# Performance work log

Hardware: AMD Instinct MI355X
Metric: run time of the kernel (lower is better)

The kernel has to match this reference:

```python
import jax, jax.numpy as jnp
import numpy as np

NUM_CLASSES = 2   # module init num_classes; class logits have NUM_CLASSES+1 (incl. 'no object')
ORIG_H, ORIG_W = 512, 512  # original input resolution that masks are upsampled to


def setup_inputs() -> dict:
    key = jax.random.key(0)
    k1, k2 = jax.random.split(key)
    B, Q = 8, 100
    h, w = 128, 128  # mask decoder outputs at 1/4 input resolution
    class_queries_logits = jax.random.normal(k1, (B, Q, NUM_CLASSES + 1), dtype=jnp.float32)
    masks_queries_logits = jax.random.normal(k2, (B, Q, h, w), dtype=jnp.float32)
    return {"class_queries_logits": class_queries_logits,
            "masks_queries_logits": masks_queries_logits}


def reference(class_queries_logits, masks_queries_logits):
    B, Q = masks_queries_logits.shape[:2]
    # bilinear upsample to original resolution (align_corners=False == half-pixel centers)
    masks_up = jax.image.resize(masks_queries_logits, (B, Q, ORIG_H, ORIG_W), method="bilinear")
    # softmax over classes (incl. no-object), keep only the first NUM_CLASSES,
    # exactly as the original loop only indexes c in range(num_classes)
    class_probs = jax.nn.softmax(class_queries_logits, axis=-1)[..., :NUM_CLASSES]  # [B,Q,C]
    mask_probs = jax.nn.sigmoid(masks_up)  # [B,Q,H,W]
    # fused replacement for the triple b/q/c Python loop of weighted accumulates
    logits = jnp.einsum("bqc,bqhw->bchw", class_probs, mask_probs)  # [B,C,H,W]
    return logits
```

## Files before the change

kernel.cpp:

```cpp
#include <hip/hip_runtime.h>
#include <math.h>

#define NB 8
#define NQ 100
#define NQH 50
#define NCP1 3
#define NC 2
#define HIN 128
#define WIN 128
#define HOUT 512
#define WOUT 512
#define QSTR (HIN * WIN)

#if __has_builtin(__builtin_amdgcn_exp2f)
#define EXP2F(x) __builtin_amdgcn_exp2f(x)
#else
#define EXP2F(x) exp2f(x)
#endif
#if __has_builtin(__builtin_amdgcn_rcpf)
#define RCPF(x) __builtin_amdgcn_rcpf(x)
#else
#define RCPF(x) (1.0f / (x))
#endif

__device__ __forceinline__ float bperm(int byteaddr, float v) {
  return __int_as_float(__builtin_amdgcn_ds_bpermute(byteaddr, __float_as_int(v)));
}

__global__ __launch_bounds__(512, 4)
void m2f_fused(const float* __restrict__ cls,
               const float* __restrict__ masks,
               float* __restrict__ out) {
  const int k   = blockIdx.x;
  const int b   = blockIdx.y;
  const int tid = threadIdx.x;

  __shared__ float2 pq[NQ];
  __shared__ float  part[16][256];

  if (tid < NQ) {
    const float* cl = cls + (b * NQ + tid) * NCP1;
    float a0 = cl[0], a1 = cl[1], a2 = cl[2];
    float mx = fmaxf(a0, fmaxf(a1, a2));
    const float L2E = 1.4426950408889634f;
    float e0 = EXP2F((a0 - mx) * L2E);
    float e1 = EXP2F((a1 - mx) * L2E);
    float e2 = EXP2F((a2 - mx) * L2E);
    float inv = RCPF(e0 + e1 + e2);
    pq[tid] = make_float2(e0 * inv, e1 * inv);
  }
  __syncthreads();

  const int wave = tid >> 6;
  const int r    = wave & 3;
  const int qh   = wave >> 2;
  const int lane = tid & 63;
  const int q0   = qh * NQH;

  const int rlo = (r < 2) ? (k > 0 ? k - 1 : 0) : k;
  const int rhi = (r < 2) ? k : (k < HIN - 1 ? k + 1 : HIN - 1);
  const float NL2E = -1.4426950408889634f;
  const float wlo = ((r == 0) ? 0.375f : (r == 1) ? 0.125f
                   : (r == 2) ? 0.875f : 0.625f) * NL2E;
  const float whi = ((r == 0) ? 0.625f : (r == 1) ? 0.875f
                   : (r == 2) ? 0.125f : 0.375f) * NL2E;

  const int oA = rlo * WIN + 2 * lane;
  const int oB = rhi * WIN + 2 * lane;
  const float* __restrict__ base = masks + (size_t)b * NQ * QSTR;

  const int addrL = (lane - 1) << 2;
  const int addrR = (lane + 1) << 2;
  const bool edgeL = (lane == 0);
  const bool edgeR = (lane == 63);

  float c0[8], c1[8];
#pragma unroll
  for (int j = 0; j < 8; ++j) { c0[j] = 0.f; c1[j] = 0.f; }

  float2 A0, B0, A1, B1, A2, B2, A3, B3;

#define LOADSET(S, qq)                                                    \
  do {                                                                    \
    const float* mq = base + (size_t)(qq) * QSTR;   \
    A##S = *(const float2*)(mq + oA);                                     \
    B##S = *(const float2*)(mq + oB);                                     \
  } while (0)

#define COMPUTE(S, qq)                                                    \
  do {                                                                    \
    const float2 pd = pq[qq];                                             \
    float t0 = fmaf(wlo, A##S.x, whi * B##S.x);             \
    float t1 = fmaf(wlo, A##S.y, whi * B##S.y);             \
    float tLr = bperm(addrL, t1);                                         \
    float tRr = bperm(addrR, t0);                                         \
    float tL = edgeL ? t0 : tLr;                                          \
    float tR = edgeR ? t1 : tRr;                                          \
    float dm = tL - t0, dd = t1 - t0, dp = tR - t1;                       \
    float v0 = fmaf(0.375f, dm, t0);                                      \
    float v1 = fmaf(0.125f, dm, t0);                                      \
    float v2 = fmaf(0.125f, dd, t0);                                      \
    float v3 = fmaf(0.375f, dd, t0);                                      \
    float v4 = fmaf(0.625f, dd, t0);                                      \
    float v5 = fmaf(0.875f, dd, t0);                                      \
    float v6 = fmaf(0.125f, dp, t1);                                      \
    float v7 = fmaf(0.375f, dp, t1);                                      \
    float s0 = RCPF(1.0f + EXP2F(v0));                                    \
    float s1 = RCPF(1.0f + EXP2F(v1));                                    \
    float s2 = RCPF(1.0f + EXP2F(v2));                                    \
    float s3 = RCPF(1.0f + EXP2F(v3));                                    \
    float s4 = RCPF(1.0f + EXP2F(v4));                                    \
    float s5 = RCPF(1.0f + EXP2F(v5));                                    \
    float s6 = RCPF(1.0f + EXP2F(v6));                                    \
    float s7 = RCPF(1.0f + EXP2F(v7));                                    \
    c0[0] = fmaf(pd.x, s0, c0[0]);  c1[0] = fmaf(pd.y, s0, c1[0]);        \
    c0[1] = fmaf(pd.x, s1, c0[1]);  c1[1] = fmaf(pd.y, s1, c1[1]);        \
    c0[2] = fmaf(pd.x, s2, c0[2]);  c1[2] = fmaf(pd.y, s2, c1[2]);        \
    c0[3] = fmaf(pd.x, s3, c0[3]);  c1[3] = fmaf(pd.y, s3, c1[3]);        \
    c0[4] = fmaf(pd.x, s4, c0[4]);  c1[4] = fmaf(pd.y, s4, c1[4]);        \
    c0[5] = fmaf(pd.x, s5, c0[5]);  c1[5] = fmaf(pd.y, s5, c1[5]);        \
    c0[6] = fmaf(pd.x, s6, c0[6]);  c1[6] = fmaf(pd.y, s6, c1[6]);        \
    c0[7] = fmaf(pd.x, s7, c0[7]);  c1[7] = fmaf(pd.y, s7, c1[7]);        \
  } while (0)

  LOADSET(0, q0); LOADSET(1, q0 + 1); LOADSET(2, q0 + 2); LOADSET(3, q0 + 3);

  for (int q = 0; q < NQH - 2; q += 4) {
    COMPUTE(0, q0 + q);     if (q + 4 < NQH) LOADSET(0, q0 + q + 4);
    COMPUTE(1, q0 + q + 1); if (q + 5 < NQH) LOADSET(1, q0 + q + 5);
    COMPUTE(2, q0 + q + 2); if (q + 6 < NQH) LOADSET(2, q0 + q + 6);
    COMPUTE(3, q0 + q + 3); if (q + 7 < NQH) LOADSET(3, q0 + q + 7);
  }
  COMPUTE(0, q0 + NQH - 2);
  COMPUTE(1, q0 + NQH - 1);

  const int col = r * 64 + lane;
  if (qh == 1) {
#pragma unroll
    for (int j = 0; j < 8; ++j) { part[j][col] = c0[j]; part[j + 8][col] = c1[j]; }
  }
  __syncthreads();
  if (qh == 0) {
#pragma unroll
    for (int j = 0; j < 8; ++j) { c0[j] += part[j][col]; c1[j] += part[j + 8][col]; }

    const int y  = 4 * k + r;
    const int x0 = 8 * lane;
    float* o0 = out + (((size_t)b * NC + 0) * HOUT + y) * WOUT + x0;
    float* o1 = out + (((size_t)b * NC + 1) * HOUT + y) * WOUT + x0;
    *(float4*)o0       = make_float4(c0[0], c0[1], c0[2], c0[3]);
    *(float4*)(o0 + 4) = make_float4(c0[4], c0[5], c0[6], c0[7]);
    *(float4*)o1       = make_float4(c1[0], c1[1], c1[2], c1[3]);
    *(float4*)(o1 + 4) = make_float4(c1[4], c1[5], c1[6], c1[7]);
  }
}

extern "C" void kernel_launch(void* const* d_in, const int* in_sizes, int n_in,
                              void* d_out, int out_size, void* d_ws, size_t ws_size,
                              hipStream_t stream) {
  const float* cls   = (const float*)d_in[0];
  const float* masks = (const float*)d_in[1];
  float* out = (float*)d_out;
  dim3 grid(HIN, NB);
  m2f_fused<<<grid, 512, 0, stream>>>(cls, masks, out);
}
```

Before: 132.9 us.

## Use inline-asm global loads with explicit vmcnt waits and 5-deep prefetch

Replaces the compiler-generated mask loads with inline-asm global_load_dwordx2 instructions that use a scalar base and a per-lane byte offset, and waits on them with explicit s_waitcnt vmcnt(8). The prefetch ring grows from 4 to 5 query slots, so more loads stay in flight and the compiler's conservative full waits are avoided. In exchange it depends on exact vmcnt counting and 32-bit offsets, and it costs extra VGPRs for the additional buffer, which could reduce occupancy.

```diff
diff --git a/kernel.cpp b/kernel.cpp
--- a/kernel.cpp
+++ b/kernel.cpp
@@ -11,6 +11,7 @@
 #define HOUT 512
 #define WOUT 512
 #define QSTR (HIN * WIN)
+#define QBYTES (QSTR * 4)
 
 #if __has_builtin(__builtin_amdgcn_exp2f)
 #define EXP2F(x) __builtin_amdgcn_exp2f(x)
@@ -65,9 +66,9 @@
   const float whi = ((r == 0) ? 0.625f : (r == 1) ? 0.875f
                    : (r == 2) ? 0.125f : 0.375f) * NL2E;
 
-  const int oA = rlo * WIN + 2 * lane;
-  const int oB = rhi * WIN + 2 * lane;
-  const float* __restrict__ base = masks + (size_t)b * NQ * QSTR;
+  const int voffA = q0 * QBYTES + (rlo * WIN + 2 * lane) * 4;
+  const int voffB = q0 * QBYTES + (rhi * WIN + 2 * lane) * 4;
+  const float* const basep = masks + (size_t)b * NQ * QSTR;
 
   const int addrL = (lane - 1) << 2;
   const int addrR = (lane + 1) << 2;
@@ -78,14 +79,19 @@
 #pragma unroll
   for (int j = 0; j < 8; ++j) { c0[j] = 0.f; c1[j] = 0.f; }
 
-  float2 A0, B0, A1, B1, A2, B2, A3, B3;
+  float2 A0, B0, A1, B1, A2, B2, A3, B3, A4, B4;
 
-#define LOADSET(S, qq)                                                    \
+#define LOADSET(S, qrel)                                                  \
   do {                                                                    \
-    const float* mq = base + (size_t)(qq) * QSTR;   \
-    A##S = *(const float2*)(mq + oA);                                     \
-    B##S = *(const float2*)(mq + oB);                                     \
+    asm volatile("global_load_dwordx2 %0, %2, %3\n\t"                     \
+                 "global_load_dwordx2 %1, %4, %3"                         \
+                 : "=&v"(A##S), "=&v"(B##S)                               \
+                 : "v"(voffA + (qrel) * QBYTES), "s"(basep),              \
+                   "v"(voffB + (qrel) * QBYTES));                         \
   } while (0)
+
+#define WAITS(S)                                                          \
+  asm volatile("s_waitcnt vmcnt(8)" : "+v"(A##S), "+v"(B##S))
 
 #define COMPUTE(S, qq)                                                    \
   do {                                                                    \
@@ -123,16 +129,24 @@
     c0[7] = fmaf(pd.x, s7, c0[7]);  c1[7] = fmaf(pd.y, s7, c1[7]);        \
   } while (0)
 
-  LOADSET(0, q0); LOADSET(1, q0 + 1); LOADSET(2, q0 + 2); LOADSET(3, q0 + 3);
+  LOADSET(0, 0); LOADSET(1, 1); LOADSET(2, 2); LOADSET(3, 3); LOADSET(4, 4);
 
-  for (int q = 0; q < NQH - 2; q += 4) {
-    COMPUTE(0, q0 + q);     if (q + 4 < NQH) LOADSET(0, q0 + q + 4);
-    COMPUTE(1, q0 + q + 1); if (q + 5 < NQH) LOADSET(1, q0 + q + 5);
-    COMPUTE(2, q0 + q + 2); if (q + 6 < NQH) LOADSET(2, q0 + q + 6);
-    COMPUTE(3, q0 + q + 3); if (q + 7 < NQH) LOADSET(3, q0 + q + 7);
+  for (int q = 0; q < NQH - 5; q += 5) {
+    WAITS(0); COMPUTE(0, q0 + q);     LOADSET(0, q + 5);
+    WAITS(1); COMPUTE(1, q0 + q + 1); LOADSET(1, q + 6);
+    WAITS(2); COMPUTE(2, q0 + q + 2); LOADSET(2, q + 7);
+    WAITS(3); COMPUTE(3, q0 + q + 3); LOADSET(3, q + 8);
+    WAITS(4); COMPUTE(4, q0 + q + 4); LOADSET(4, q + 9);
   }
-  COMPUTE(0, q0 + NQH - 2);
-  COMPUTE(1, q0 + NQH - 1);
+
+  asm volatile("s_waitcnt vmcnt(0)"
+               : "+v"(A0), "+v"(B0), "+v"(A1), "+v"(B1), "+v"(A2), "+v"(B2),
+                 "+v"(A3), "+v"(B3), "+v"(A4), "+v"(B4));
+  COMPUTE(0, q0 + NQH - 5);
+  COMPUTE(1, q0 + NQH - 4);
+  COMPUTE(2, q0 + NQH - 3);
+  COMPUTE(3, q0 + NQH - 2);
+  COMPUTE(4, q0 + NQH - 1);
 
   const int col = r * 64 + lane;
   if (qh == 1) {
```

After: 129.9 us. 2.2% less time.
